# Optimization experiments

Hardware: AMD Instinct MI355X
Metric: run time of the kernel (lower is better)

## Reference

```python
import jax, jax.numpy as jnp
import numpy as np

B, C, Dz, Hh, Ww = 1, 128, 24, 24, 24
L = Dz * Hh * Ww
D_STATE = 16
D_CONV = 4
EXPAND = 2
D_INNER = EXPAND * C
DT_RANK = (C + 15) // 16  # ceil(d_model/16) = 8


def setup_inputs() -> dict:
    key = jax.random.key(0)
    ks = jax.random.split(key, 10)
    s = 0.02
    return {
        "x": jax.random.normal(ks[0], (B, C, Dz, Hh, Ww), dtype=jnp.float32),
        "ln_w": jnp.ones((C,), jnp.float32),
        "ln_b": jnp.zeros((C,), jnp.float32),
        "in_proj_w": s * jax.random.normal(ks[1], (2 * D_INNER, C), jnp.float32),
        "conv_w": s * jax.random.normal(ks[2], (D_INNER, D_CONV), jnp.float32),
        "conv_b": jnp.zeros((D_INNER,), jnp.float32),
        "x_proj_w": s * jax.random.normal(ks[3], (DT_RANK + 2 * D_STATE, D_INNER), jnp.float32),
        "dt_proj_w": s * jax.random.normal(ks[4], (D_INNER, DT_RANK), jnp.float32),
        "dt_proj_b": jax.random.uniform(ks[5], (D_INNER,), jnp.float32, -4.0, -2.0),
        "A_log": jnp.log(jnp.broadcast_to(jnp.arange(1, D_STATE + 1, dtype=jnp.float32), (D_INNER, D_STATE))),
        "D_param": jnp.ones((D_INNER,), jnp.float32),
        "out_proj_w": s * jax.random.normal(ks[6], (C, D_INNER), jnp.float32),
    }


def _mamba_forward(x, ln_w, ln_b, in_proj_w, conv_w, conv_b, x_proj_w,
                   dt_proj_w, dt_proj_b, A_log, D_param, out_proj_w):
    b, c, d, h, w = x.shape
    l = d * h * w
    tokens = x.reshape(b, c, l).transpose(0, 2, 1)  # (B,L,C)

    # LayerNorm over channel dim
    mu = jnp.mean(tokens, axis=-1, keepdims=True)
    var = jnp.var(tokens, axis=-1, keepdims=True)
    tn = (tokens - mu) * jax.lax.rsqrt(var + 1e-5) * ln_w + ln_b

    # in_proj -> x, z
    xz = jnp.einsum('blc,ec->ble', tn, in_proj_w)  # (B,L,2*d_inner)
    xs, z = jnp.split(xz, 2, axis=-1)

    # causal depthwise conv1d over L (kernel size D_CONV)
    xpad = jnp.pad(xs, ((0, 0), (D_CONV - 1, 0), (0, 0)))
    xc = conv_b
    xc = sum(xpad[:, k:k + l, :] * conv_w[:, k] for k in range(D_CONV)) + conv_b
    xa = jax.nn.silu(xc)  # (B,L,d_inner)

    # x_proj -> dt, B, C
    x_dbl = jnp.einsum('bld,ed->ble', xa, x_proj_w)
    dt_in = x_dbl[..., :DT_RANK]
    Bm = x_dbl[..., DT_RANK:DT_RANK + D_STATE]          # (B,L,d_state)
    Cm = x_dbl[..., DT_RANK + D_STATE:]                 # (B,L,d_state)
    dt = jax.nn.softplus(jnp.einsum('blr,dr->bld', dt_in, dt_proj_w) + dt_proj_b)

    A = -jnp.exp(A_log)  # (d_inner, d_state)

    def step(hst, inp):
        dt_t, B_t, C_t, x_t = inp  # (B,d_inner),(B,d_state),(B,d_state),(B,d_inner)
        dA = jnp.exp(dt_t[..., None] * A)                       # (B,d_inner,d_state)
        hst = dA * hst + (dt_t * x_t)[..., None] * B_t[:, None, :]
        y_t = jnp.einsum('bds,bs->bd', hst, C_t)
        return hst, y_t

    h0 = jnp.zeros((b, D_INNER, D_STATE), xa.dtype)
    xs_t = (dt.transpose(1, 0, 2), Bm.transpose(1, 0, 2), Cm.transpose(1, 0, 2), xa.transpose(1, 0, 2))
    _, ys = jax.lax.scan(step, h0, xs_t)
    y = ys.transpose(1, 0, 2) + xa * D_param  # (B,L,d_inner)

    y = y * jax.nn.silu(z)
    out = jnp.einsum('bld,cd->blc', y, out_proj_w)

    tokens = tokens + out
    return tokens.transpose(0, 2, 1).reshape(b, c, d, h, w)


def reference(x, ln_w, ln_b, in_proj_w, conv_w, conv_b, x_proj_w,
              dt_proj_w, dt_proj_b, A_log, D_param, out_proj_w):
    return _mamba_forward(x, ln_w, ln_b, in_proj_w, conv_w, conv_b, x_proj_w,
                          dt_proj_w, dt_proj_b, A_log, D_param, out_proj_w)
```

## Files before the change

### kernel.cpp

```cpp
#include <hip/hip_runtime.h>
#include <hip/hip_bf16.h>
#include <math.h>


constexpr int LQ = 13824;
constexpr int NC = 108;
constexpr int CH = 128;
constexpr int DI = 256;
constexpr int DS = 16;

typedef __attribute__((ext_vector_type(8))) short short8v;
typedef __attribute__((ext_vector_type(4))) float float4v;

__device__ __forceinline__ ushort f2bf(float f) {
  uint u = __float_as_uint(f);
  u += 0x7FFFu + ((u >> 16) & 1u);
  return (ushort)(u >> 16);
}
__device__ __forceinline__ float bf2f(ushort u) {
  return __uint_as_float(((uint)u) << 16);
}

template<int CTRL>
__device__ __forceinline__ float dpp_add(float x) {
  int y = __builtin_amdgcn_update_dpp(0, __float_as_int(x), CTRL, 0xF, 0xF, true);
  return x + __int_as_float(y);
}

__global__ __launch_bounds__(256) void prep_w(const float* __restrict__ w_in,
    const float* __restrict__ w_xp, const float* __restrict__ w_out,
    ushort* __restrict__ b_in, ushort* __restrict__ b_xp, ushort* __restrict__ b_out) {
  int idx = blockIdx.x * 256 + threadIdx.x;
  if (idx < 512 * 128) {
    b_in[idx] = f2bf(w_in[idx]);
  } else if (idx < 512 * 128 + 64 * 256) {
    int j = idx - 512 * 128; int r = j >> 8, k = j & 255;
    b_xp[j] = (r < 40) ? f2bf(w_xp[r * 256 + k]) : (ushort)0;
  } else if (idx < 512 * 128 + 64 * 256 + 128 * 256) {
    int j = idx - (512 * 128 + 64 * 256);
    b_out[j] = f2bf(w_out[j]);
  }
}

__global__ __launch_bounds__(256) void ln_t(const float* __restrict__ x,
    const float* __restrict__ lnw, const float* __restrict__ lnb,
    ushort* __restrict__ tn) {
  __shared__ float red[64][8];
  __shared__ float stat[64][2];
  __shared__ ushort T[64][136];
  const int t = threadIdx.x;
  const int l = t & 63, q = t >> 6;
  const int l0 = blockIdx.x * 64;
  float sum = 0.f, sq = 0.f;
  #pragma unroll 8
  for (int cc = 0; cc < 32; ++cc) {
    int c = q * 32 + cc;
    float v = x[(size_t)c * LQ + l0 + l];
    sum += v; sq += v * v;
  }
  red[l][q] = sum; red[l][4 + q] = sq;
  __syncthreads();
  if (t < 64) {
    float s  = red[t][0] + red[t][1] + red[t][2] + red[t][3];
    float s2 = red[t][4] + red[t][5] + red[t][6] + red[t][7];
    float mu = s * (1.f / 128.f);
    float var = s2 * (1.f / 128.f) - mu * mu;
    stat[t][0] = mu; stat[t][1] = rsqrtf(var + 1e-5f);
  }
  __syncthreads();
  float mu = stat[l][0], rs = stat[l][1];
  #pragma unroll 8
  for (int cc = 0; cc < 32; ++cc) {
    int c = q * 32 + cc;
    float v = x[(size_t)c * LQ + l0 + l];
    T[l][c] = f2bf((v - mu) * rs * lnw[c] + lnb[c]);
  }
  __syncthreads();
  int row = t >> 2, seg = t & 3;
  #pragma unroll
  for (int j = 0; j < 4; ++j) {
    short8v v = *(const short8v*)&T[row][seg * 32 + j * 8];
    *(short8v*)&tn[(size_t)(l0 + row) * 128 + seg * 32 + j * 8] = v;
  }
}

template<int K, int MV, int BSTR, int CSTR>
__global__ __launch_bounds__(256) void gemm_tok(
    const ushort* __restrict__ Wb,
    const ushort* __restrict__ Act,
    ushort* __restrict__ Out) {
  constexpr int KO = K / 8;
  __shared__ ushort As[64 * K];
  __shared__ ushort Bs[128 * 64];
  const int tid = threadIdx.x;
  const int l0 = blockIdx.x * 128;
  const int m0 = blockIdx.y * 64;
  #pragma unroll
  for (int i = 0; i < (64 * KO) / 256; ++i) {
    int cid = i * 256 + tid;
    int m = cid / KO, oct = cid % KO;
    short8v v = *(const short8v*)&Wb[(size_t)(m0 + m) * K + oct * 8];
    *(short8v*)&As[m * K + ((oct ^ (m & 7)) * 8)] = v;
  }
  float4v acc[4][2];
  #pragma unroll
  for (int a = 0; a < 4; ++a)
    #pragma unroll
    for (int b = 0; b < 2; ++b) acc[a][b] = (float4v)0.f;
  const int w = tid >> 6, lane = tid & 63;
  const int r = lane & 15, g = lane >> 4;
  for (int k0 = 0; k0 < K; k0 += 64) {
    __syncthreads();
    #pragma unroll
    for (int i = 0; i < 4; ++i) {
      int cid = i * 256 + tid;
      int l = cid >> 3, oct = cid & 7;
      short8v v = *(const short8v*)&Act[(size_t)(l0 + l) * BSTR + k0 + oct * 8];
      *(short8v*)&Bs[l * 64 + ((oct ^ (l & 7)) * 8)] = v;
    }
    __syncthreads();
    #pragma unroll
    for (int kk = 0; kk < 2; ++kk) {
      short8v af[4], bfv[2];
      int ko = (k0 >> 3) + kk * 4 + g;
      #pragma unroll
      for (int mf = 0; mf < 4; ++mf) {
        int row = mf * 16 + r;
        af[mf] = *(const short8v*)&As[row * K + ((ko ^ (row & 7)) * 8)];
      }
      int kob = kk * 4 + g;
      #pragma unroll
      for (int nf = 0; nf < 2; ++nf) {
        int row = w * 32 + nf * 16 + r;
        bfv[nf] = *(const short8v*)&Bs[row * 64 + ((kob ^ (row & 7)) * 8)];
      }
      #pragma unroll
      for (int mf = 0; mf < 4; ++mf)
        #pragma unroll
        for (int nf = 0; nf < 2; ++nf)
          acc[mf][nf] = __builtin_amdgcn_mfma_f32_16x16x32_bf16(af[mf], bfv[nf], acc[mf][nf], 0, 0, 0);
    }
  }
  __syncthreads();
  #pragma unroll
  for (int mf = 0; mf < 4; ++mf) {
    #pragma unroll
    for (int nf = 0; nf < 2; ++nf) {
      int l = w * 32 + nf * 16 + r;
      int m = mf * 16 + g * 4;
      ushort u0 = f2bf(acc[mf][nf][0]), u1 = f2bf(acc[mf][nf][1]);
      ushort u2 = f2bf(acc[mf][nf][2]), u3 = f2bf(acc[mf][nf][3]);
      uint2 pk = make_uint2((uint)u0 | ((uint)u1 << 16), (uint)u2 | ((uint)u3 << 16));
      int oct = (m >> 3) ^ (l & 7);
      *(uint2*)&Bs[l * 64 + oct * 8 + (g & 1) * 4] = pk;
    }
  }
  __syncthreads();
  #pragma unroll
  for (int i = 0; i < 4; ++i) {
    int cid = i * 256 + tid;
    int row = cid >> 3, oct = cid & 7;
    if (oct * 8 < MV) {
      short8v v = *(const short8v*)&Bs[row * 64 + ((oct ^ (row & 7)) * 8)];
      *(short8v*)&Out[(size_t)(l0 + row) * CSTR + m0 + oct * 8] = v;
    }
  }
}

__global__ __launch_bounds__(256) void gemm_out_k(
    const ushort* __restrict__ Wb,
    const ushort* __restrict__ Yg,
    const float* __restrict__ X,
    float* __restrict__ Out) {
  __shared__ ushort Ay[128 * 64];
  __shared__ ushort Bw[128 * 64];
  const int tid = threadIdx.x;
  const int l0 = blockIdx.x * 128;
  const int w = tid >> 6, lane = tid & 63;
  const int r = lane & 15, g = lane >> 4;
  const int lw = w >> 1, cw = w & 1;
  float4v acc[4][4];
  #pragma unroll
  for (int a = 0; a < 4; ++a)
    #pragma unroll
    for (int b = 0; b < 4; ++b) acc[a][b] = (float4v)0.f;
  for (int k0 = 0; k0 < 256; k0 += 64) {
    __syncthreads();
    #pragma unroll
    for (int i = 0; i < 4; ++i) {
      int cid = i * 256 + tid;
      int row = cid >> 3, oct = cid & 7;
      int k = k0 + oct * 8;
      int slab = k >> 4, rem = k & 15;
      short8v va = *(const short8v*)&Yg[((size_t)slab * LQ + l0 + row) * 16 + rem];
      *(short8v*)&Ay[row * 64 + ((oct ^ (row & 7)) * 8)] = va;
      short8v vb = *(const short8v*)&Wb[(size_t)row * 256 + k0 + oct * 8];
      *(short8v*)&Bw[row * 64 + ((oct ^ (row & 7)) * 8)] = vb;
    }
    __syncthreads();
    #pragma unroll
    for (int kk = 0; kk < 2; ++kk) {
      int ko = kk * 4 + g;
      short8v af[4], bfv[4];
      #pragma unroll
      for (int mf = 0; mf < 4; ++mf) {
        int row = lw * 64 + mf * 16 + r;
        af[mf] = *(const short8v*)&Ay[row * 64 + ((ko ^ (row & 7)) * 8)];
      }
      #pragma unroll
      for (int nf = 0; nf < 4; ++nf) {
        int row = cw * 64 + nf * 16 + r;
        bfv[nf] = *(const short8v*)&Bw[row * 64 + ((ko ^ (row & 7)) * 8)];
      }
      #pragma unroll
      for (int mf = 0; mf < 4; ++mf)
        #pragma unroll
        for (int nf = 0; nf < 4; ++nf)
          acc[mf][nf] = __builtin_amdgcn_mfma_f32_16x16x32_bf16(af[mf], bfv[nf], acc[mf][nf], 0, 0, 0);
    }
  }
  #pragma unroll
  for (int mf = 0; mf < 4; ++mf) {
    #pragma unroll
    for (int nf = 0; nf < 4; ++nf) {
      int c = cw * 64 + nf * 16 + r;
      int l = l0 + lw * 64 + mf * 16 + g * 4;
      size_t off = (size_t)c * LQ + l;
      float4 rv = *(const float4*)&X[off];
      float4 o = make_float4(acc[mf][nf][0] + rv.x, acc[mf][nf][1] + rv.y,
                             acc[mf][nf][2] + rv.z, acc[mf][nf][3] + rv.w);
      *(float4*)&Out[off] = o;
    }
  }
}

__global__ __launch_bounds__(256) void conv_silu_t(const ushort* __restrict__ xz,
    const float* __restrict__ cw, const float* __restrict__ cb,
    ushort* __restrict__ xa) {
  const int l = blockIdx.x, d = threadIdx.x;
  float4 wv = *(const float4*)&cw[d * 4];
  float acc = cb[d];
  if (l >= 3) acc += bf2f(xz[(size_t)(l - 3) * 512 + d]) * wv.x;
  if (l >= 2) acc += bf2f(xz[(size_t)(l - 2) * 512 + d]) * wv.y;
  if (l >= 1) acc += bf2f(xz[(size_t)(l - 1) * 512 + d]) * wv.z;
  acc += bf2f(xz[(size_t)l * 512 + d]) * wv.w;
  xa[(size_t)l * 256 + d] = f2bf(acc / (1.f + __expf(-acc)));
}

__global__ __launch_bounds__(256) void dtproj_t(const ushort* __restrict__ xdbl,
    const float* __restrict__ Wdt, const float* __restrict__ bias,
    ushort* __restrict__ dt) {
  const int l = blockIdx.x, d = threadIdx.x;
  float acc = bias[d];
  #pragma unroll
  for (int rr = 0; rr < 8; ++rr)
    acc += Wdt[d * 8 + rr] * bf2f(xdbl[(size_t)l * 48 + rr]);
  float sp = (acc > 20.f) ? acc : log1pf(__expf(acc));
  dt[(size_t)l * 256 + d] = f2bf(sp);
}

__global__ __launch_bounds__(256) void scan_pass1_t(const ushort* __restrict__ dtg,
    const ushort* __restrict__ xag, const ushort* __restrict__ xdbl,
    const float* __restrict__ A_log, float* __restrict__ Pc, float* __restrict__ Hc) {
  __shared__ float du[128][36];
  __shared__ float Bsh[128][16];
  const int tid = threadIdx.x;
  const int c = blockIdx.x, dg = blockIdx.y;
  const int l0 = c * CH;
  {
    int row = tid >> 1, half = tid & 1;
    const size_t gb = (size_t)(l0 + row) * 256 + dg * 16 + half * 8;
    short8v dv = *(const short8v*)&dtg[gb];
    short8v xv = *(const short8v*)&xag[gb];
    float o[16];
    #pragma unroll
    for (int j = 0; j < 8; ++j) {
      float dtf = bf2f((ushort)dv[j]);
      o[j * 2] = dtf; o[j * 2 + 1] = dtf * bf2f((ushort)xv[j]);
    }
    #pragma unroll
    for (int j = 0; j < 4; ++j)
      *(float4*)&du[row][half * 16 + j * 4] =
          make_float4(o[j * 4], o[j * 4 + 1], o[j * 4 + 2], o[j * 4 + 3]);
    if (tid < 128) {
      short8v b0 = *(const short8v*)&xdbl[(size_t)(l0 + tid) * 48 + 8];
      short8v b1 = *(const short8v*)&xdbl[(size_t)(l0 + tid) * 48 + 16];
      #pragma unroll
      for (int j = 0; j < 8; ++j) {
        Bsh[tid][j] = bf2f((ushort)b0[j]);
        Bsh[tid][8 + j] = bf2f((ushort)b1[j]);
      }
    }
  }
  __syncthreads();
  const int s = tid & 15, dloc = tid >> 4;
  const int d = dg * 16 + dloc;
  const float A = -__expf(A_log[d * DS + s]);
  float p = 1.f, h = 0.f;
  #pragma unroll 4
  for (int i = 0; i < CH; ++i) {
    float dtv = du[i][dloc * 2], dx = du[i][dloc * 2 + 1];
    float a = __expf(dtv * A);
    p *= a;
    h = fmaf(a, h, dx * Bsh[i][s]);
  }
  int idx = (c * DI + d) * DS + s;
  Pc[idx] = p; Hc[idx] = h;
}

__global__ __launch_bounds__(256) void scan_combine(const float* __restrict__ Pc,
    const float* __restrict__ Hc, float* __restrict__ Hin) {
  int t = blockIdx.x * 256 + threadIdx.x;
  float h = 0.f;
  for (int c = 0; c < NC; ++c) {
    Hin[c * 4096 + t] = h;
    h = Pc[c * 4096 + t] * h + Hc[c * 4096 + t];
  }
}

__global__ __launch_bounds__(256) void scan_pass2_t(const ushort* __restrict__ dtg,
    const ushort* __restrict__ xag, const ushort* __restrict__ xdbl,
    const ushort* __restrict__ xz, const float* __restrict__ A_log,
    const float* __restrict__ Dp, const float* __restrict__ Hin,
    ushort* __restrict__ yg) {
  __shared__ float du[128][36];
  __shared__ float bc[128][36];
  __shared__ float ylds[128][20];
  const int tid = threadIdx.x;
  const int c = blockIdx.x, dg = blockIdx.y;
  const int l0 = c * CH;
  {
    int row = tid >> 1, half = tid & 1;
    const size_t gb = (size_t)(l0 + row) * 256 + dg * 16 + half * 8;
    short8v dv = *(const short8v*)&dtg[gb];
    short8v xv = *(const short8v*)&xag[gb];
    float o[16];
    #pragma unroll
    for (int j = 0; j < 8; ++j) {
      float dtf = bf2f((ushort)dv[j]);
      o[j * 2] = dtf; o[j * 2 + 1] = dtf * bf2f((ushort)xv[j]);
    }
    #pragma unroll
    for (int j = 0; j < 4; ++j)
      *(float4*)&du[row][half * 16 + j * 4] =
          make_float4(o[j * 4], o[j * 4 + 1], o[j * 4 + 2], o[j * 4 + 3]);
    if (tid < 128) {
      const size_t xb = (size_t)(l0 + tid) * 48;
      short8v b0 = *(const short8v*)&xdbl[xb + 8];
      short8v b1 = *(const short8v*)&xdbl[xb + 16];
      short8v c0 = *(const short8v*)&xdbl[xb + 24];
      short8v c1 = *(const short8v*)&xdbl[xb + 32];
      #pragma unroll
      for (int j = 0; j < 8; ++j) {
        bc[tid][j * 2]           = bf2f((ushort)b0[j]);
        bc[tid][j * 2 + 1]       = bf2f((ushort)c0[j]);
        bc[tid][16 + j * 2]      = bf2f((ushort)b1[j]);
        bc[tid][16 + j * 2 + 1]  = bf2f((ushort)c1[j]);
      }
    }
  }
  __syncthreads();
  const int s = tid & 15, dloc = tid >> 4;
  const int d = dg * 16 + dloc;
  const float A = -__expf(A_log[d * DS + s]);
  float h = Hin[c * 4096 + d * DS + s];
  #pragma unroll 4
  for (int i = 0; i < CH; ++i) {
    float dtv = du[i][dloc * 2], dx = du[i][dloc * 2 + 1];
    float Bv = bc[i][s * 2], Cv = bc[i][s * 2 + 1];
    float a = __expf(dtv * A);
    h = fmaf(a, h, dx * Bv);
    float t = h * Cv;
    t = dpp_add<0xB1>(t);
    t = dpp_add<0x4E>(t);
    t = dpp_add<0x141>(t);
    t = dpp_add<0x140>(t);
    if (s == 0) ylds[i][dloc] = t;
  }
  __syncthreads();
  if (tid < 128) {
    int row = tid;
    const size_t gxa = (size_t)(l0 + row) * 256 + dg * 16;
    const size_t gz  = (size_t)(l0 + row) * 512 + 256 + dg * 16;
    short8v xv0 = *(const short8v*)&xag[gxa];
    short8v xv1 = *(const short8v*)&xag[gxa + 8];
    short8v zv0 = *(const short8v*)&xz[gz];
    short8v zv1 = *(const short8v*)&xz[gz + 8];
    ushort o[16];
    #pragma unroll
    for (int j = 0; j < 16; ++j) {
      float yv = ylds[row][j];
      float xf = bf2f((ushort)(j < 8 ? xv0[j] : xv1[j - 8]));
      float zf = bf2f((ushort)(j < 8 ? zv0[j] : zv1[j - 8]));
      float val = (yv + xf * Dp[dg * 16 + j]) * (zf / (1.f + __expf(-zf)));
      o[j] = f2bf(val);
    }
    ushort* dst = &yg[((size_t)dg * LQ + l0 + row) * 16];
    #pragma unroll
    for (int j = 0; j < 8; ++j) {
      ((ushort*)dst)[j] = o[j];
      ((ushort*)dst)[8 + j] = o[8 + j];
    }
  }
}

extern "C" void kernel_launch(void* const* d_in, const int* in_sizes, int n_in,
                              void* d_out, int out_size, void* d_ws, size_t ws_size,
                              hipStream_t stream) {
  const float* x         = (const float*)d_in[0];
  const float* ln_w      = (const float*)d_in[1];
  const float* ln_b      = (const float*)d_in[2];
  const float* in_proj_w = (const float*)d_in[3];
  const float* conv_w    = (const float*)d_in[4];
  const float* conv_b    = (const float*)d_in[5];
  const float* x_proj_w  = (const float*)d_in[6];
  const float* dt_proj_w = (const float*)d_in[7];
  const float* dt_proj_b = (const float*)d_in[8];
  const float* A_log     = (const float*)d_in[9];
  const float* D_param   = (const float*)d_in[10];
  const float* out_proj_w= (const float*)d_in[11];
  float* out = (float*)d_out;

  char* ws = (char*)d_ws;
  ushort* wbf_in  = (ushort*)(ws + 0);
  ushort* wbf_xp  = (ushort*)(ws + 131072);
  ushort* wbf_out = (ushort*)(ws + 163840);
  ushort* tn_t    = (ushort*)(ws + 229376);
  ushort* xz_t    = (ushort*)(ws + 3768320);
  ushort* xa_t    = (ushort*)(ws + 17924096);
  ushort* xdbl_t  = (ushort*)(ws + 25001984);
  ushort* dt_t    = (ushort*)(ws + 26329088);
  ushort* yg_t    = (ushort*)(ws + 33406976);
  float*  Pc      = (float*)(ws + 40484864);
  float*  Hc      = (float*)(ws + 42254336);
  float*  Hin     = (float*)(ws + 44023808);

  prep_w<<<448, 256, 0, stream>>>(in_proj_w, x_proj_w, out_proj_w, wbf_in, wbf_xp, wbf_out);
  ln_t<<<LQ / 64, 256, 0, stream>>>(x, ln_w, ln_b, tn_t);
  gemm_tok<128, 64, 128, 512><<<dim3(NC, 8), 256, 0, stream>>>(wbf_in, tn_t, xz_t);
  conv_silu_t<<<LQ, 256, 0, stream>>>(xz_t, conv_w, conv_b, xa_t);
  gemm_tok<256, 40, 256, 48><<<dim3(NC, 1), 256, 0, stream>>>(wbf_xp, xa_t, xdbl_t);
  dtproj_t<<<LQ, 256, 0, stream>>>(xdbl_t, dt_proj_w, dt_proj_b, dt_t);
  scan_pass1_t<<<dim3(NC, 16), 256, 0, stream>>>(dt_t, xa_t, xdbl_t, A_log, Pc, Hc);
  scan_combine<<<16, 256, 0, stream>>>(Pc, Hc, Hin);
  scan_pass2_t<<<dim3(NC, 16), 256, 0, stream>>>(dt_t, xa_t, xdbl_t, xz_t, A_log, D_param, Hin, yg_t);
  gemm_out_k<<<NC, 256, 0, stream>>>(wbf_out, yg_t, x, out);
}
```

Measured before the change: 203.8 us.

## Fold dt_proj into x_proj GEMM and split scan into local plus carry-in correction

Precomputes W_dt·W_xp so the x_proj GEMM directly emits the 256 dt pre-activations alongside B and C, which removes the separate dtproj kernel and its dt buffer. Scan pass 1 now also computes the chunk-local y with zero initial state. Pass 2 then only adds a carry-in correction, hin·exp(A·cumsum dt)·C, before applying the D skip term and the z gate. The conv kernel is vectorised so each thread handles 8 channels over 4 tokens, and LDS staging is packed as bf16. The trade-offs are a larger GEMM N dimension (320), bf16 rounding of dt, dx and B/C in shared memory, and a fused weight product that changes rounding.

```diff
diff --git a/kernel.cpp b/kernel.cpp
--- a/kernel.cpp
+++ b/kernel.cpp
@@ -26,18 +26,34 @@
   int y = __builtin_amdgcn_update_dpp(0, __float_as_int(x), CTRL, 0xF, 0xF, true);
   return x + __int_as_float(y);
 }
-
-__global__ __launch_bounds__(256) void prep_w(const float* __restrict__ w_in,
-    const float* __restrict__ w_xp, const float* __restrict__ w_out,
-    ushort* __restrict__ b_in, ushort* __restrict__ b_xp, ushort* __restrict__ b_out) {
+__device__ __forceinline__ float dpp_reduce16(float t) {
+  t = dpp_add<0xB1>(t);
+  t = dpp_add<0x4E>(t);
+  t = dpp_add<0x141>(t);
+  t = dpp_add<0x140>(t);
+  return t;
+}
+
+__global__ __launch_bounds__(256) void prep_w2(const float* __restrict__ w_in,
+    const float* __restrict__ w_xp, const float* __restrict__ w_dt,
+    const float* __restrict__ w_out,
+    ushort* __restrict__ b_in, ushort* __restrict__ b_xp2, ushort* __restrict__ b_out) {
   int idx = blockIdx.x * 256 + threadIdx.x;
-  if (idx < 512 * 128) {
+  if (idx < 65536) {
     b_in[idx] = f2bf(w_in[idx]);
-  } else if (idx < 512 * 128 + 64 * 256) {
-    int j = idx - 512 * 128; int r = j >> 8, k = j & 255;
-    b_xp[j] = (r < 40) ? f2bf(w_xp[r * 256 + k]) : (ushort)0;
-  } else if (idx < 512 * 128 + 64 * 256 + 128 * 256) {
-    int j = idx - (512 * 128 + 64 * 256);
+  } else if (idx < 65536 + 8192) {
+    int j = idx - 65536; int r = j >> 8, k = j & 255;
+    b_xp2[j] = f2bf(w_xp[(8 + r) * 256 + k]);
+  } else if (idx < 65536 + 8192 + 65536) {
+    int j = idx - (65536 + 8192); int d = j >> 8, k = j & 255;
+    float acc = 0.f;
+    #pragma unroll
+    for (int r = 0; r < 8; ++r) acc += w_dt[d * 8 + r] * w_xp[r * 256 + k];
+    b_xp2[8192 + j] = f2bf(acc);
+  } else if (idx < 65536 + 8192 + 65536 + 8192) {
+    b_xp2[73728 + (idx - 139264)] = 0;
+  } else if (idx < 180224) {
+    int j = idx - 147456;
     b_out[j] = f2bf(w_out[j]);
   }
 }
@@ -234,62 +250,76 @@
   }
 }
 
-__global__ __launch_bounds__(256) void conv_silu_t(const ushort* __restrict__ xz,
+__global__ __launch_bounds__(256) void conv2(const ushort* __restrict__ xz,
     const float* __restrict__ cw, const float* __restrict__ cb,
     ushort* __restrict__ xa) {
-  const int l = blockIdx.x, d = threadIdx.x;
-  float4 wv = *(const float4*)&cw[d * 4];
-  float acc = cb[d];
-  if (l >= 3) acc += bf2f(xz[(size_t)(l - 3) * 512 + d]) * wv.x;
-  if (l >= 2) acc += bf2f(xz[(size_t)(l - 2) * 512 + d]) * wv.y;
-  if (l >= 1) acc += bf2f(xz[(size_t)(l - 1) * 512 + d]) * wv.z;
-  acc += bf2f(xz[(size_t)l * 512 + d]) * wv.w;
-  xa[(size_t)l * 256 + d] = f2bf(acc / (1.f + __expf(-acc)));
-}
-
-__global__ __launch_bounds__(256) void dtproj_t(const ushort* __restrict__ xdbl,
-    const float* __restrict__ Wdt, const float* __restrict__ bias,
-    ushort* __restrict__ dt) {
-  const int l = blockIdx.x, d = threadIdx.x;
-  float acc = bias[d];
-  #pragma unroll
-  for (int rr = 0; rr < 8; ++rr)
-    acc += Wdt[d * 8 + rr] * bf2f(xdbl[(size_t)l * 48 + rr]);
-  float sp = (acc > 20.f) ? acc : log1pf(__expf(acc));
-  dt[(size_t)l * 256 + d] = f2bf(sp);
-}
-
-__global__ __launch_bounds__(256) void scan_pass1_t(const ushort* __restrict__ dtg,
-    const ushort* __restrict__ xag, const ushort* __restrict__ xdbl,
-    const float* __restrict__ A_log, float* __restrict__ Pc, float* __restrict__ Hc) {
-  __shared__ float du[128][36];
-  __shared__ float Bsh[128][16];
+  const int tid = threadIdx.x;
+  const int d0 = (tid & 31) * 8;
+  const int l0 = blockIdx.x * 32 + (tid >> 5) * 4;
+  float w0[8], w1[8], w2[8], w3[8], bb[8];
+  #pragma unroll
+  for (int j = 0; j < 8; ++j) {
+    float4 wv = *(const float4*)&cw[(d0 + j) * 4];
+    w0[j] = wv.x; w1[j] = wv.y; w2[j] = wv.z; w3[j] = wv.w;
+    bb[j] = cb[d0 + j];
+  }
+  float rbuf[7][8];
+  #pragma unroll
+  for (int t = 0; t < 7; ++t) {
+    int ls = l0 - 3 + t;
+    if (ls >= 0) {
+      short8v v = *(const short8v*)&xz[(size_t)ls * 512 + d0];
+      #pragma unroll
+      for (int j = 0; j < 8; ++j) rbuf[t][j] = bf2f((ushort)v[j]);
+    } else {
+      #pragma unroll
+      for (int j = 0; j < 8; ++j) rbuf[t][j] = 0.f;
+    }
+  }
+  #pragma unroll
+  for (int i = 0; i < 4; ++i) {
+    short8v ov;
+    #pragma unroll
+    for (int j = 0; j < 8; ++j) {
+      float acc = bb[j] + w0[j] * rbuf[i][j] + w1[j] * rbuf[i + 1][j]
+                        + w2[j] * rbuf[i + 2][j] + w3[j] * rbuf[i + 3][j];
+      ov[j] = (short)f2bf(acc / (1.f + __expf(-acc)));
+    }
+    *(short8v*)&xa[(size_t)(l0 + i) * 256 + d0] = ov;
+  }
+}
+
+__global__ __launch_bounds__(256) void scan1(const ushort* __restrict__ xdbl,
+    const ushort* __restrict__ xa, const float* __restrict__ bias,
+    const float* __restrict__ A_log, float* __restrict__ Pc, float* __restrict__ Hc,
+    ushort* __restrict__ yloc) {
+  __shared__ uint  duL[128 * 17];
+  __shared__ ushort bcL[128 * 40];
+  __shared__ float ylds[128 * 18];
   const int tid = threadIdx.x;
   const int c = blockIdx.x, dg = blockIdx.y;
   const int l0 = c * CH;
   {
-    int row = tid >> 1, half = tid & 1;
-    const size_t gb = (size_t)(l0 + row) * 256 + dg * 16 + half * 8;
-    short8v dv = *(const short8v*)&dtg[gb];
-    short8v xv = *(const short8v*)&xag[gb];
-    float o[16];
+    const int row = tid >> 1, half = tid & 1;
+    const ushort* xr = xdbl + (size_t)(l0 + row) * 320;
+    short8v dl = *(const short8v*)(xr + 32 + dg * 16 + half * 8);
+    short8v xv = *(const short8v*)(&xa[(size_t)(l0 + row) * 256 + dg * 16 + half * 8]);
     #pragma unroll
     for (int j = 0; j < 8; ++j) {
-      float dtf = bf2f((ushort)dv[j]);
-      o[j * 2] = dtf; o[j * 2 + 1] = dtf * bf2f((ushort)xv[j]);
-    }
-    #pragma unroll
-    for (int j = 0; j < 4; ++j)
-      *(float4*)&du[row][half * 16 + j * 4] =
-          make_float4(o[j * 4], o[j * 4 + 1], o[j * 4 + 2], o[j * 4 + 3]);
-    if (tid < 128) {
-      short8v b0 = *(const short8v*)&xdbl[(size_t)(l0 + tid) * 48 + 8];
-      short8v b1 = *(const short8v*)&xdbl[(size_t)(l0 + tid) * 48 + 16];
-      #pragma unroll
-      for (int j = 0; j < 8; ++j) {
-        Bsh[tid][j] = bf2f((ushort)b0[j]);
-        Bsh[tid][8 + j] = bf2f((ushort)b1[j]);
-      }
+      float av = bf2f((ushort)dl[j]) + bias[dg * 16 + half * 8 + j];
+      float sp = (av > 20.f) ? av : log1pf(__expf(av));
+      float dx = sp * bf2f((ushort)xv[j]);
+      duL[row * 17 + half * 8 + j] = (uint)f2bf(sp) | ((uint)f2bf(dx) << 16);
+    }
+    short8v bv = *(const short8v*)(xr + half * 8);
+    short8v cv = *(const short8v*)(xr + 16 + half * 8);
+    uint* bcu = (uint*)bcL;
+    #pragma unroll
+    for (int j = 0; j < 4; ++j) {
+      bcu[row * 20 + half * 4 + j] =
+          (uint)(ushort)bv[2 * j] | ((uint)(ushort)bv[2 * j + 1] << 16);
+      bcu[row * 20 + 8 + half * 4 + j] =
+          (uint)(ushort)cv[2 * j] | ((uint)(ushort)cv[2 * j + 1] << 16);
     }
   }
   __syncthreads();
@@ -299,13 +329,25 @@
   float p = 1.f, h = 0.f;
   #pragma unroll 4
   for (int i = 0; i < CH; ++i) {
-    float dtv = du[i][dloc * 2], dx = du[i][dloc * 2 + 1];
+    uint pv = duL[i * 17 + dloc];
+    float dtv = bf2f((ushort)(pv & 0xffffu));
+    float dx  = bf2f((ushort)(pv >> 16));
     float a = __expf(dtv * A);
     p *= a;
-    h = fmaf(a, h, dx * Bsh[i][s]);
+    h = fmaf(a, h, dx * bf2f(bcL[i * 40 + s]));
+    float t = dpp_reduce16(h * bf2f(bcL[i * 40 + 16 + s]));
+    if (s == 0) ylds[i * 18 + dloc] = t;
   }
   int idx = (c * DI + d) * DS + s;
   Pc[idx] = p; Hc[idx] = h;
+  __syncthreads();
+  {
+    const int row = tid >> 1, half = tid & 1;
+    short8v ov;
+    #pragma unroll
+    for (int j = 0; j < 8; ++j) ov[j] = (short)f2bf(ylds[row * 18 + half * 8 + j]);
+    *(short8v*)&yloc[((size_t)dg * LQ + l0 + row) * 16 + half * 8] = ov;
+  }
 }
 
 __global__ __launch_bounds__(256) void scan_combine(const float* __restrict__ Pc,
@@ -318,89 +360,68 @@
   }
 }
 
-__global__ __launch_bounds__(256) void scan_pass2_t(const ushort* __restrict__ dtg,
-    const ushort* __restrict__ xag, const ushort* __restrict__ xdbl,
-    const ushort* __restrict__ xz, const float* __restrict__ A_log,
+__global__ __launch_bounds__(256) void scan2(const ushort* __restrict__ xdbl,
+    const ushort* __restrict__ xa, const ushort* __restrict__ xz,
+    const float* __restrict__ bias, const float* __restrict__ A_log,
     const float* __restrict__ Dp, const float* __restrict__ Hin,
     ushort* __restrict__ yg) {
-  __shared__ float du[128][36];
-  __shared__ float bc[128][36];
-  __shared__ float ylds[128][20];
+  __shared__ ushort dtL[128 * 18];
+  __shared__ ushort cL[128 * 18];
+  __shared__ float corr[128 * 18];
   const int tid = threadIdx.x;
   const int c = blockIdx.x, dg = blockIdx.y;
   const int l0 = c * CH;
   {
-    int row = tid >> 1, half = tid & 1;
-    const size_t gb = (size_t)(l0 + row) * 256 + dg * 16 + half * 8;
-    short8v dv = *(const short8v*)&dtg[gb];
-    short8v xv = *(const short8v*)&xag[gb];
-    float o[16];
+    const int row = tid >> 1, half = tid & 1;
+    const ushort* xr = xdbl + (size_t)(l0 + row) * 320;
+    short8v dl = *(const short8v*)(xr + 32 + dg * 16 + half * 8);
+    short8v cv = *(const short8v*)(xr + 16 + half * 8);
+    uint* dtu = (uint*)dtL;
+    uint* cu  = (uint*)cL;
+    ushort sp8[8];
     #pragma unroll
     for (int j = 0; j < 8; ++j) {
-      float dtf = bf2f((ushort)dv[j]);
-      o[j * 2] = dtf; o[j * 2 + 1] = dtf * bf2f((ushort)xv[j]);
-    }
-    #pragma unroll
-    for (int j = 0; j < 4; ++j)
-      *(float4*)&du[row][half * 16 + j * 4] =
-          make_float4(o[j * 4], o[j * 4 + 1], o[j * 4 + 2], o[j * 4 + 3]);
-    if (tid < 128) {
-      const size_t xb = (size_t)(l0 + tid) * 48;
-      short8v b0 = *(const short8v*)&xdbl[xb + 8];
-      short8v b1 = *(const short8v*)&xdbl[xb + 16];
-      short8v c0 = *(const short8v*)&xdbl[xb + 24];
-      short8v c1 = *(const short8v*)&xdbl[xb + 32];
-      #pragma unroll
-      for (int j = 0; j < 8; ++j) {
-        bc[tid][j * 2]           = bf2f((ushort)b0[j]);
-        bc[tid][j * 2 + 1]       = bf2f((ushort)c0[j]);
-        bc[tid][16 + j * 2]      = bf2f((ushort)b1[j]);
-        bc[tid][16 + j * 2 + 1]  = bf2f((ushort)c1[j]);
-      }
+      float av = bf2f((ushort)dl[j]) + bias[dg * 16 + half * 8 + j];
+      float sp = (av > 20.f) ? av : log1pf(__expf(av));
+      sp8[j] = f2bf(sp);
+    }
+    #pragma unroll
+    for (int j = 0; j < 4; ++j) {
+      dtu[row * 9 + half * 4 + j] = (uint)sp8[2 * j] | ((uint)sp8[2 * j + 1] << 16);
+      cu[row * 9 + half * 4 + j] =
+          (uint)(ushort)cv[2 * j] | ((uint)(ushort)cv[2 * j + 1] << 16);
     }
   }
   __syncthreads();
   const int s = tid & 15, dloc = tid >> 4;
   const int d = dg * 16 + dloc;
   const float A = -__expf(A_log[d * DS + s]);
-  float h = Hin[c * 4096 + d * DS + s];
+  const float hin = Hin[c * 4096 + d * DS + s];
+  float S = 0.f;
   #pragma unroll 4
   for (int i = 0; i < CH; ++i) {
-    float dtv = du[i][dloc * 2], dx = du[i][dloc * 2 + 1];
-    float Bv = bc[i][s * 2], Cv = bc[i][s * 2 + 1];
-    float a = __expf(dtv * A);
-    h = fmaf(a, h, dx * Bv);
-    float t = h * Cv;
-    t = dpp_add<0xB1>(t);
-    t = dpp_add<0x4E>(t);
-    t = dpp_add<0x141>(t);
-    t = dpp_add<0x140>(t);
-    if (s == 0) ylds[i][dloc] = t;
-  }
-  __syncthreads();
-  if (tid < 128) {
-    int row = tid;
-    const size_t gxa = (size_t)(l0 + row) * 256 + dg * 16;
-    const size_t gz  = (size_t)(l0 + row) * 512 + 256 + dg * 16;
-    short8v xv0 = *(const short8v*)&xag[gxa];
-    short8v xv1 = *(const short8v*)&xag[gxa + 8];
-    short8v zv0 = *(const short8v*)&xz[gz];
-    short8v zv1 = *(const short8v*)&xz[gz + 8];
-    ushort o[16];
-    #pragma unroll
-    for (int j = 0; j < 16; ++j) {
-      float yv = ylds[row][j];
-      float xf = bf2f((ushort)(j < 8 ? xv0[j] : xv1[j - 8]));
-      float zf = bf2f((ushort)(j < 8 ? zv0[j] : zv1[j - 8]));
-      float val = (yv + xf * Dp[dg * 16 + j]) * (zf / (1.f + __expf(-zf)));
-      o[j] = f2bf(val);
-    }
-    ushort* dst = &yg[((size_t)dg * LQ + l0 + row) * 16];
+    S += bf2f(dtL[i * 18 + dloc]);
+    float e = __expf(A * S);
+    float t = dpp_reduce16((hin * e) * bf2f(cL[i * 18 + s]));
+    if (s == 0) corr[i * 18 + dloc] = t;
+  }
+  __syncthreads();
+  {
+    const int row = tid >> 1, half = tid & 1;
+    const size_t slab = ((size_t)dg * LQ + l0 + row) * 16 + half * 8;
+    short8v yl = *(const short8v*)&yg[slab];
+    short8v xv = *(const short8v*)&xa[(size_t)(l0 + row) * 256 + dg * 16 + half * 8];
+    short8v zv = *(const short8v*)&xz[(size_t)(l0 + row) * 512 + 256 + dg * 16 + half * 8];
+    short8v ov;
     #pragma unroll
     for (int j = 0; j < 8; ++j) {
-      ((ushort*)dst)[j] = o[j];
-      ((ushort*)dst)[8 + j] = o[8 + j];
-    }
+      float val = bf2f((ushort)yl[j]) + corr[row * 18 + half * 8 + j]
+                + bf2f((ushort)xv[j]) * Dp[dg * 16 + half * 8 + j];
+      float zf = bf2f((ushort)zv[j]);
+      val *= zf / (1.f + __expf(-zf));
+      ov[j] = (short)f2bf(val);
+    }
+    *(short8v*)&yg[slab] = ov;
   }
 }
 
@@ -423,26 +444,26 @@
 
   char* ws = (char*)d_ws;
   ushort* wbf_in  = (ushort*)(ws + 0);
-  ushort* wbf_xp  = (ushort*)(ws + 131072);
-  ushort* wbf_out = (ushort*)(ws + 163840);
-  ushort* tn_t    = (ushort*)(ws + 229376);
-  ushort* xz_t    = (ushort*)(ws + 3768320);
-  ushort* xa_t    = (ushort*)(ws + 17924096);
-  ushort* xdbl_t  = (ushort*)(ws + 25001984);
-  ushort* dt_t    = (ushort*)(ws + 26329088);
-  ushort* yg_t    = (ushort*)(ws + 33406976);
-  float*  Pc      = (float*)(ws + 40484864);
-  float*  Hc      = (float*)(ws + 42254336);
-  float*  Hin     = (float*)(ws + 44023808);
-
-  prep_w<<<448, 256, 0, stream>>>(in_proj_w, x_proj_w, out_proj_w, wbf_in, wbf_xp, wbf_out);
+  ushort* wbf_xp2 = (ushort*)(ws + 131072);
+  ushort* wbf_out = (ushort*)(ws + 294912);
+  float*  Hin     = (float*)(ws + 360448);
+  ushort* tn_t    = (ushort*)(ws + 2129920);
+  float*  Pc      = (float*)(ws + 2129920);
+  float*  Hc      = (float*)(ws + 3899392);
+  ushort* xz_t    = (ushort*)(ws + 5668864);
+  ushort* xa_t    = (ushort*)(ws + 19824640);
+  ushort* xdbl_t  = (ushort*)(ws + 26902528);
+  ushort* yg_t    = (ushort*)(ws + 35749888);
+
+  prep_w2<<<704, 256, 0, stream>>>(in_proj_w, x_proj_w, dt_proj_w, out_proj_w,
+                                   wbf_in, wbf_xp2, wbf_out);
   ln_t<<<LQ / 64, 256, 0, stream>>>(x, ln_w, ln_b, tn_t);
   gemm_tok<128, 64, 128, 512><<<dim3(NC, 8), 256, 0, stream>>>(wbf_in, tn_t, xz_t);
-  conv_silu_t<<<LQ, 256, 0, stream>>>(xz_t, conv_w, conv_b, xa_t);
-  gemm_tok<256, 40, 256, 48><<<dim3(NC, 1), 256, 0, stream>>>(wbf_xp, xa_t, xdbl_t);
-  dtproj_t<<<LQ, 256, 0, stream>>>(xdbl_t, dt_proj_w, dt_proj_b, dt_t);
-  scan_pass1_t<<<dim3(NC, 16), 256, 0, stream>>>(dt_t, xa_t, xdbl_t, A_log, Pc, Hc);
+  conv2<<<LQ / 32, 256, 0, stream>>>(xz_t, conv_w, conv_b, xa_t);
+  gemm_tok<256, 64, 256, 320><<<dim3(NC, 5), 256, 0, stream>>>(wbf_xp2, xa_t, xdbl_t);
+  scan1<<<dim3(NC, 16), 256, 0, stream>>>(xdbl_t, xa_t, dt_proj_b, A_log, Pc, Hc, yg_t);
   scan_combine<<<16, 256, 0, stream>>>(Pc, Hc, Hin);
-  scan_pass2_t<<<dim3(NC, 16), 256, 0, stream>>>(dt_t, xa_t, xdbl_t, xz_t, A_log, D_param, Hin, yg_t);
+  scan2<<<dim3(NC, 16), 256, 0, stream>>>(xdbl_t, xa_t, xz_t, dt_proj_b, A_log,
+                                          D_param, Hin, yg_t);
   gemm_out_k<<<NC, 256, 0, stream>>>(wbf_out, yg_t, x, out);
 }
```

Result: no change. 207.2 us (+1.6%).
